# Performance work log

Hardware: AMD Instinct MI355X
Metric: run time of the kernel (lower is better)

## Reference

```python
import jax, jax.numpy as jnp
import numpy as np

NUM_USERS = 300_000
NUM_ITEMS = 200_000
N = NUM_USERS + NUM_ITEMS
DIM = 64
E = 2_500_000
NUM_LAYERS = 4
EMB_STD = 0.01


def setup_inputs() -> dict:
    key = jax.random.key(0)
    k1, k2, k3 = jax.random.split(key, 3)
    edge_index = jax.random.randint(k1, (2, E), 0, N, dtype=jnp.int32)
    emb_users = EMB_STD * jax.random.normal(k2, (NUM_USERS, DIM), dtype=jnp.float32)
    emb_items = EMB_STD * jax.random.normal(k3, (NUM_ITEMS, DIM), dtype=jnp.float32)
    return {"edge_index": edge_index, "emb_users": emb_users, "emb_items": emb_items}


def reference(edge_index, emb_users, emb_items):
    row, col = edge_index[0], edge_index[1]  # source, target
    x = jnp.concatenate([emb_users, emb_items], axis=0)  # [N, D]

    # gcn_norm (LGConv: no self loops): deg over target, sym normalization
    deg = jax.ops.segment_sum(jnp.ones((E,), x.dtype), col, num_segments=N)  # [N]
    deg_inv_sqrt = jnp.where(deg > 0, jax.lax.rsqrt(jnp.maximum(deg, 1.0)), 0.0)
    norm = deg_inv_sqrt[row] * deg_inv_sqrt[col]  # [E]

    embs = [x]
    for _ in range(NUM_LAYERS):
        # out[col] += norm * x[row]  (edge-wise gather, scale, scatter-add)
        x = jax.ops.segment_sum(norm[:, None] * x[row], col, num_segments=N)
        embs.append(x)

    # faithful to source: extra 1/(L+1) factor on top of the mean
    emb_final = (1.0 / (NUM_LAYERS + 1)) * jnp.mean(jnp.stack(embs, axis=1), axis=1)
    emb_users_final = emb_final[:NUM_USERS]
    emb_items_final = emb_final[NUM_USERS:]
    return (emb_users_final, emb_users, emb_items_final, emb_items)
```

## Files before the change

### kernel.cpp

```cpp
#include <hip/hip_runtime.h>
#include <stdint.h>

#define U_CNT 300000
#define I_CNT 200000
#define N_CNT 500000
#define DIM 64
#define SCAN_CHUNK 1024
#define NB1 ((N_CNT + SCAN_CHUNK - 1) / SCAN_CHUNK)

typedef unsigned short bf16_t;

__device__ __forceinline__ float lof(uint32_t u) { return __uint_as_float(u << 16); }
__device__ __forceinline__ float hif(uint32_t u) { return __uint_as_float(u & 0xFFFF0000u); }
__device__ __forceinline__ uint32_t rnd_bf(float f) {
    uint32_t u = __float_as_uint(f);
    return u + (0x7FFFu + ((u >> 16) & 1u));
}
__device__ __forceinline__ uint32_t packbf(float lo, float hi) {
    return (rnd_bf(lo) >> 16) | (rnd_bf(hi) & 0xFFFF0000u);
}
__device__ __forceinline__ bf16_t f2b(float f) { return (bf16_t)(rnd_bf(f) >> 16); }


__global__ void deg_cnt_kernel(const int* __restrict__ col, int* __restrict__ cnt, int E) {
    int e = blockIdx.x * blockDim.x + threadIdx.x;
    if (e < E) atomicAdd(&cnt[col[e]], 1);
}

__global__ void dis_kernel(const int* __restrict__ cnt, float* __restrict__ dis, int n) {
    int i = blockIdx.x * blockDim.x + threadIdx.x;
    if (i < n) {
        int d = cnt[i];
        dis[i] = d > 0 ? rsqrtf((float)d) : 0.0f;
    }
}


__global__ void scan1_kernel(const int* __restrict__ cnt, int* __restrict__ bsum, int n) {
    __shared__ int lds[256];
    int t = threadIdx.x;
    int i = blockIdx.x * SCAN_CHUNK + t * 4;
    int4 v = make_int4(0, 0, 0, 0);
    if (i + 3 < n) v = *(const int4*)(cnt + i);
    else {
        if (i     < n) v.x = cnt[i];
        if (i + 1 < n) v.y = cnt[i + 1];
        if (i + 2 < n) v.z = cnt[i + 2];
        if (i + 3 < n) v.w = cnt[i + 3];
    }
    lds[t] = v.x + v.y + v.z + v.w;
    __syncthreads();
    for (int o = 128; o > 0; o >>= 1) {
        if (t < o) lds[t] += lds[t + o];
        __syncthreads();
    }
    if (t == 0) bsum[blockIdx.x] = lds[0];
}

__global__ void scan2_kernel(int* __restrict__ bsum, int nb) {
    __shared__ int lds[512];
    int t = threadIdx.x;
    int v = (t < nb) ? bsum[t] : 0;
    lds[t] = v;
    __syncthreads();
    for (int o = 1; o < 512; o <<= 1) {
        int a = lds[t] + ((t >= o) ? lds[t - o] : 0);
        __syncthreads();
        lds[t] = a;
        __syncthreads();
    }
    if (t < nb) bsum[t] = lds[t] - v;
}

__global__ void scan3_kernel(const int* __restrict__ cnt, const int* __restrict__ bsum,
                             int* __restrict__ off, int* __restrict__ cur, int n, int E) {
    __shared__ int lds[256];
    int t = threadIdx.x;
    int i = blockIdx.x * SCAN_CHUNK + t * 4;
    int4 v = make_int4(0, 0, 0, 0);
    if (i + 3 < n) v = *(const int4*)(cnt + i);
    else {
        if (i     < n) v.x = cnt[i];
        if (i + 1 < n) v.y = cnt[i + 1];
        if (i + 2 < n) v.z = cnt[i + 2];
        if (i + 3 < n) v.w = cnt[i + 3];
    }
    int s = v.x + v.y + v.z + v.w;
    lds[t] = s;
    __syncthreads();
    for (int o = 1; o < 256; o <<= 1) {
        int a = lds[t] + ((t >= o) ? lds[t - o] : 0);
        __syncthreads();
        lds[t] = a;
        __syncthreads();
    }
    int ex = lds[t] - s + bsum[blockIdx.x];
    int o0 = ex, o1 = ex + v.x, o2 = o1 + v.y, o3 = o2 + v.z;
    if (i     < n) { off[i]     = o0; cur[i]     = o0; }
    if (i + 1 < n) { off[i + 1] = o1; cur[i + 1] = o1; }
    if (i + 2 < n) { off[i + 2] = o2; cur[i + 2] = o2; }
    if (i + 3 < n) { off[i + 3] = o3; cur[i + 3] = o3; }
    if (i == n - 4) off[n] = E;
}

__global__ void fill_kernel(const int* __restrict__ row, const int* __restrict__ col,
                            const float* __restrict__ dis, int* __restrict__ cur,
                            int2* __restrict__ csr, int E) {
    int e = blockIdx.x * blockDim.x + threadIdx.x;
    if (e < E) {
        int r = row[e], c = col[e];
        int p = atomicAdd(&cur[c], 1);
        int2 pr;
        pr.x = r;
        pr.y = __float_as_int(dis[r] * dis[c]);
        csr[p] = pr;
    }
}


__global__ void f2b_kernel(const float4* __restrict__ src, ushort4* __restrict__ dst, int n4) {
    int i = blockIdx.x * blockDim.x + threadIdx.x;
    if (i < n4) {
        float4 v = src[i];
        ushort4 w;
        w.x = f2b(v.x); w.y = f2b(v.y); w.z = f2b(v.z); w.w = f2b(v.w);
        dst[i] = w;
    }
}

__global__ __launch_bounds__(256) void gather8_kernel(
        const int* __restrict__ off, const int2* __restrict__ csr,
        const uint32_t* __restrict__ xb, uint4* __restrict__ yb, int nE) {
    int lane = threadIdx.x & 63;
    int sub  = lane & 7;
    int n = blockIdx.x * 32 + (threadIdx.x >> 6) * 8 + (lane >> 3);
    int s = off[n], e = off[n + 1];
    const uint4* xv = (const uint4*)xb;

    float a0 = 0, a1 = 0, a2 = 0, a3 = 0, a4 = 0, a5 = 0, a6 = 0, a7 = 0;

    int i0 = s;
    int2 pa = csr[(i0     < nE) ? i0     : (nE - 1)];
    int2 pb = csr[(i0 + 1 < nE) ? i0 + 1 : (nE - 1)];
    float na = (i0     < e) ? __int_as_float(pa.y) : 0.0f;
    float nb = (i0 + 1 < e) ? __int_as_float(pb.y) : 0.0f;
    int   ra = (i0     < e) ? pa.x : 0;
    int   rb = (i0 + 1 < e) ? pb.x : 0;
    uint4 va = xv[((size_t)ra << 3) + sub];
    uint4 vb = xv[((size_t)rb << 3) + sub];
    int i1 = i0 + 2;
    int2 qa = csr[(i1     < nE) ? i1     : (nE - 1)];
    int2 qb = csr[(i1 + 1 < nE) ? i1 + 1 : (nE - 1)];

    while (i0 < e) {
        float ma = (i1     < e) ? __int_as_float(qa.y) : 0.0f;
        float mb = (i1 + 1 < e) ? __int_as_float(qb.y) : 0.0f;
        int   sa = (i1     < e) ? qa.x : 0;
        int   sb = (i1 + 1 < e) ? qb.x : 0;
        uint4 wa = xv[((size_t)sa << 3) + sub];
        uint4 wb = xv[((size_t)sb << 3) + sub];
        int i2 = i1 + 2;
        qa = csr[(i2     < nE) ? i2     : (nE - 1)];
        qb = csr[(i2 + 1 < nE) ? i2 + 1 : (nE - 1)];
        a0 = fmaf(na, lof(va.x), a0); a1 = fmaf(na, hif(va.x), a1);
        a2 = fmaf(na, lof(va.y), a2); a3 = fmaf(na, hif(va.y), a3);
        a4 = fmaf(na, lof(va.z), a4); a5 = fmaf(na, hif(va.z), a5);
        a6 = fmaf(na, lof(va.w), a6); a7 = fmaf(na, hif(va.w), a7);
        a0 = fmaf(nb, lof(vb.x), a0); a1 = fmaf(nb, hif(vb.x), a1);
        a2 = fmaf(nb, lof(vb.y), a2); a3 = fmaf(nb, hif(vb.y), a3);
        a4 = fmaf(nb, lof(vb.z), a4); a5 = fmaf(nb, hif(vb.z), a5);
        a6 = fmaf(nb, lof(vb.w), a6); a7 = fmaf(nb, hif(vb.w), a7);
        va = wa; vb = wb; na = ma; nb = mb;
        i0 = i1; i1 = i2;
    }

    uint4 w;
    w.x = packbf(a0, a1); w.y = packbf(a2, a3);
    w.z = packbf(a4, a5); w.w = packbf(a6, a7);
    yb[((size_t)n << 3) + sub] = w;
}

__global__ __launch_bounds__(256) void gather_final_kernel(
        const int* __restrict__ off, const int2* __restrict__ csr,
        const uint32_t* __restrict__ xb,
        const uint4* __restrict__ y1, const uint4* __restrict__ y2,
        const float* __restrict__ embU, const float* __restrict__ embIadj,
        float* __restrict__ finU, float* __restrict__ finIadj,
        float* __restrict__ cpyU, float* __restrict__ cpyIadj, int nE) {
    int lane = threadIdx.x & 63;
    int sub  = lane & 7;
    int n = blockIdx.x * 32 + (threadIdx.x >> 6) * 8 + (lane >> 3);
    int s = off[n], e = off[n + 1];
    const uint4* xv = (const uint4*)xb;

    size_t nodeOff = ((size_t)n << 3) + sub;
    size_t fbase   = ((size_t)n << 6) + (size_t)sub * 8;
    const float* embP = (n < U_CNT ? embU : embIadj) + fbase;
    float*       finP = (n < U_CNT ? finU : finIadj) + fbase;
    float*       cpyP = (n < U_CNT ? cpyU : cpyIadj) + fbase;
    float4 b0 = *(const float4*)embP;
    float4 b1 = *(const float4*)(embP + 4);
    uint4 u1 = y1[nodeOff];
    uint4 u2 = y2[nodeOff];
    uint4 u3 = xv[nodeOff];

    float a0 = 0, a1 = 0, a2 = 0, a3 = 0, a4 = 0, a5 = 0, a6 = 0, a7 = 0;

    int i0 = s;
    int2 pa = csr[(i0     < nE) ? i0     : (nE - 1)];
    int2 pb = csr[(i0 + 1 < nE) ? i0 + 1 : (nE - 1)];
    float na = (i0     < e) ? __int_as_float(pa.y) : 0.0f;
    float nb = (i0 + 1 < e) ? __int_as_float(pb.y) : 0.0f;
    int   ra = (i0     < e) ? pa.x : 0;
    int   rb = (i0 + 1 < e) ? pb.x : 0;
    uint4 va = xv[((size_t)ra << 3) + sub];
    uint4 vb = xv[((size_t)rb << 3) + sub];
    int i1 = i0 + 2;
    int2 qa = csr[(i1     < nE) ? i1     : (nE - 1)];
    int2 qb = csr[(i1 + 1 < nE) ? i1 + 1 : (nE - 1)];

    while (i0 < e) {
        float ma = (i1     < e) ? __int_as_float(qa.y) : 0.0f;
        float mb = (i1 + 1 < e) ? __int_as_float(qb.y) : 0.0f;
        int   sa = (i1     < e) ? qa.x : 0;
        int   sb = (i1 + 1 < e) ? qb.x : 0;
        uint4 wa = xv[((size_t)sa << 3) + sub];
        uint4 wb = xv[((size_t)sb << 3) + sub];
        int i2 = i1 + 2;
        qa = csr[(i2     < nE) ? i2     : (nE - 1)];
        qb = csr[(i2 + 1 < nE) ? i2 + 1 : (nE - 1)];
        a0 = fmaf(na, lof(va.x), a0); a1 = fmaf(na, hif(va.x), a1);
        a2 = fmaf(na, lof(va.y), a2); a3 = fmaf(na, hif(va.y), a3);
        a4 = fmaf(na, lof(va.z), a4); a5 = fmaf(na, hif(va.z), a5);
        a6 = fmaf(na, lof(va.w), a6); a7 = fmaf(na, hif(va.w), a7);
        a0 = fmaf(nb, lof(vb.x), a0); a1 = fmaf(nb, hif(vb.x), a1);
        a2 = fmaf(nb, lof(vb.y), a2); a3 = fmaf(nb, hif(vb.y), a3);
        a4 = fmaf(nb, lof(vb.z), a4); a5 = fmaf(nb, hif(vb.z), a5);
        a6 = fmaf(nb, lof(vb.w), a6); a7 = fmaf(nb, hif(vb.w), a7);
        va = wa; vb = wb; na = ma; nb = mb;
        i0 = i1; i1 = i2;
    }

    const float k = 1.0f / 25.0f;
    float4 r0, r1;
    r0.x = (b0.x + lof(u1.x) + lof(u2.x) + lof(u3.x) + a0) * k;
    r0.y = (b0.y + hif(u1.x) + hif(u2.x) + hif(u3.x) + a1) * k;
    r0.z = (b0.z + lof(u1.y) + lof(u2.y) + lof(u3.y) + a2) * k;
    r0.w = (b0.w + hif(u1.y) + hif(u2.y) + hif(u3.y) + a3) * k;
    r1.x = (b1.x + lof(u1.z) + lof(u2.z) + lof(u3.z) + a4) * k;
    r1.y = (b1.y + hif(u1.z) + hif(u2.z) + hif(u3.z) + a5) * k;
    r1.z = (b1.z + lof(u1.w) + lof(u2.w) + lof(u3.w) + a6) * k;
    r1.w = (b1.w + hif(u1.w) + hif(u2.w) + hif(u3.w) + a7) * k;
    *(float4*)finP = r0;
    *(float4*)(finP + 4) = r1;
    *(float4*)cpyP = b0;
    *(float4*)(cpyP + 4) = b1;
}


extern "C" void kernel_launch(void* const* d_in, const int* in_sizes, int n_in,
                              void* d_out, int out_size, void* d_ws, size_t ws_size,
                              hipStream_t stream) {
    const int*   edge = (const int*)d_in[0];
    const float* embU = (const float*)d_in[1];
    const float* embI = (const float*)d_in[2];
    const int E = in_sizes[0] / 2;
    const int* row = edge;
    const int* col = edge + E;

    float* out  = (float*)d_out;
    float* finU = out;
    float* cu   = out + (size_t)U_CNT * DIM;
    float* finI = out + (size_t)2 * U_CNT * DIM;
    float* ci   = finI + (size_t)I_CNT * DIM;

    const size_t XB = (size_t)N_CNT * DIM * sizeof(bf16_t);
    char* ws = (char*)d_ws;
    size_t p = 0;
    bf16_t* x0 = (bf16_t*)(ws + p); p += XB;
    bf16_t* y1 = (bf16_t*)(ws + p); p += XB;
    bf16_t* y2 = (bf16_t*)(ws + p); p += XB;
    bf16_t* y3 = (bf16_t*)(ws + p); p += XB;
    int*   cnt  = (int*)(ws + p);   p += ((size_t)N_CNT + 4) * sizeof(int);
    int*   off  = (int*)(ws + p);   p += ((size_t)N_CNT + 4) * sizeof(int);
    int*   cur  = (int*)(ws + p);   p += ((size_t)N_CNT + 4) * sizeof(int);
    float* dis  = (float*)(ws + p); p += ((size_t)N_CNT + 4) * sizeof(float);
    int*   bsum = (int*)(ws + p);   p += 1024 * sizeof(int);
    int2*  csr  = (int2*)(ws + p);  p += (size_t)E * sizeof(int2);

    const float* embIadj = embI - (size_t)U_CNT * DIM;
    float* finIadj = finI - (size_t)U_CNT * DIM;
    float* ciadj   = ci   - (size_t)U_CNT * DIM;

    const int B = 256;
    const int nU4 = U_CNT * DIM / 4;
    const int nI4 = I_CNT * DIM / 4;
    const int gU4 = (nU4 + B - 1) / B;
    const int gI4 = (nI4 + B - 1) / B;
    const int gE  = (E + B - 1) / B;
    const int gN  = (N_CNT + B - 1) / B;
    const int gGather = N_CNT / 32;

    hipMemsetAsync(cnt, 0, (size_t)N_CNT * sizeof(int), stream);
    deg_cnt_kernel<<<gE, B, 0, stream>>>(col, cnt, E);
    dis_kernel<<<gN, B, 0, stream>>>(cnt, dis, N_CNT);

    scan1_kernel<<<NB1, 256, 0, stream>>>(cnt, bsum, N_CNT);
    scan2_kernel<<<1, 512, 0, stream>>>(bsum, NB1);
    scan3_kernel<<<NB1, 256, 0, stream>>>(cnt, bsum, off, cur, N_CNT, E);
    fill_kernel<<<gE, B, 0, stream>>>(row, col, dis, cur, csr, E);

    f2b_kernel<<<gU4, B, 0, stream>>>((const float4*)embU, (ushort4*)x0, nU4);
    f2b_kernel<<<gI4, B, 0, stream>>>((const float4*)embI,
                                      (ushort4*)(x0 + (size_t)U_CNT * DIM), nI4);

    gather8_kernel<<<gGather, B, 0, stream>>>(off, csr, (const uint32_t*)x0, (uint4*)y1, E);
    gather8_kernel<<<gGather, B, 0, stream>>>(off, csr, (const uint32_t*)y1, (uint4*)y2, E);
    gather8_kernel<<<gGather, B, 0, stream>>>(off, csr, (const uint32_t*)y2, (uint4*)y3, E);
    gather_final_kernel<<<gGather, B, 0, stream>>>(off, csr, (const uint32_t*)y3,
        (const uint4*)y1, (const uint4*)y2,
        embU, embIadj, finU, finIadj, cu, ciadj, E);
}
```

Baseline: 599.2 us.

## Factor symmetric norm into node scaling, shrink CSR to indices, fuse setup kernels

Rewrites propagation in pre-scaled form w = D^-1/2 x, so the edge list stores only source indices (4 B instead of 8 B per edge) and each layer applies a single per-node dis^2 scale after accumulation. The dis computation is folded into the scan kernel, and the CSR fill is merged with the bf16 conversion into one launch. The embedding copies are spread across the first two layer kernels, and the third layer writes a partial layer sum so the final kernel reads one buffer instead of three. The cost is an extra bf16 workspace buffer, extra rounding from storing scaled intermediates in bf16, and nontemporal loads and stores used throughout.

Measured after the change: 735.7 us. 1.23x slower.

```diff
diff --git a/kernel.cpp b/kernel.cpp
--- a/kernel.cpp
+++ b/kernel.cpp
@@ -9,6 +9,8 @@
 #define NB1 ((N_CNT + SCAN_CHUNK - 1) / SCAN_CHUNK)
 
 typedef unsigned short bf16_t;
+typedef float    f32x4 __attribute__((ext_vector_type(4)));
+typedef uint32_t u32x4 __attribute__((ext_vector_type(4)));
 
 __device__ __forceinline__ float lof(uint32_t u) { return __uint_as_float(u << 16); }
 __device__ __forceinline__ float hif(uint32_t u) { return __uint_as_float(u & 0xFFFF0000u); }
@@ -27,16 +29,10 @@
     if (e < E) atomicAdd(&cnt[col[e]], 1);
 }
 
-__global__ void dis_kernel(const int* __restrict__ cnt, float* __restrict__ dis, int n) {
-    int i = blockIdx.x * blockDim.x + threadIdx.x;
-    if (i < n) {
-        int d = cnt[i];
-        dis[i] = d > 0 ? rsqrtf((float)d) : 0.0f;
-    }
-}
-
-
-__global__ void scan1_kernel(const int* __restrict__ cnt, int* __restrict__ bsum, int n) {
+
+__global__ void scan1_dis_kernel(const int* __restrict__ cnt, int* __restrict__ bsum,
+                                 float* __restrict__ dis, float* __restrict__ dis2,
+                                 float* __restrict__ rdis, int n) {
     __shared__ int lds[256];
     int t = threadIdx.x;
     int i = blockIdx.x * SCAN_CHUNK + t * 4;
@@ -47,6 +43,25 @@
         if (i + 1 < n) v.y = cnt[i + 1];
         if (i + 2 < n) v.z = cnt[i + 2];
         if (i + 3 < n) v.w = cnt[i + 3];
+    }
+    if (i + 3 < n) {
+        int dd[4] = {v.x, v.y, v.z, v.w};
+        f32x4 fd, f2, fr;
+        #pragma unroll
+        for (int k = 0; k < 4; k++) {
+            float d = (float)dd[k];
+            float s = dd[k] > 0 ? rsqrtf(d) : 0.0f;
+            fd[k] = s; f2[k] = s * s; fr[k] = d * s;
+        }
+        *(f32x4*)(dis + i) = fd;
+        *(f32x4*)(dis2 + i) = f2;
+        *(f32x4*)(rdis + i) = fr;
+    } else {
+        for (int k = 0; k < 4 && i + k < n; k++) {
+            int d = (&v.x)[k];
+            float s = d > 0 ? rsqrtf((float)d) : 0.0f;
+            dis[i + k] = s; dis2[i + k] = s * s; rdis[i + k] = (float)d * s;
+        }
     }
     lds[t] = v.x + v.y + v.z + v.w;
     __syncthreads();
@@ -103,60 +118,78 @@
     if (i == n - 4) off[n] = E;
 }
 
-__global__ void fill_kernel(const int* __restrict__ row, const int* __restrict__ col,
-                            const float* __restrict__ dis, int* __restrict__ cur,
-                            int2* __restrict__ csr, int E) {
-    int e = blockIdx.x * blockDim.x + threadIdx.x;
-    if (e < E) {
-        int r = row[e], c = col[e];
-        int p = atomicAdd(&cur[c], 1);
-        int2 pr;
-        pr.x = r;
-        pr.y = __float_as_int(dis[r] * dis[c]);
-        csr[p] = pr;
-    }
-}
-
-
-__global__ void f2b_kernel(const float4* __restrict__ src, ushort4* __restrict__ dst, int n4) {
-    int i = blockIdx.x * blockDim.x + threadIdx.x;
-    if (i < n4) {
-        float4 v = src[i];
+
+__global__ void fill_w0_kernel(const int* __restrict__ row, const int* __restrict__ col,
+                               int* __restrict__ cur, int* __restrict__ csr, int E, int gE,
+                               const float* __restrict__ embU, const float* __restrict__ embIadj,
+                               const float* __restrict__ dis, ushort4* __restrict__ w0) {
+    int b = blockIdx.x;
+    if (b < gE) {
+        int e = b * blockDim.x + threadIdx.x;
+        if (e < E) {
+            int r = row[e], c = col[e];
+            int p = atomicAdd(&cur[c], 1);
+            csr[p] = r;
+        }
+    } else {
+        int q = (b - gE) * blockDim.x + threadIdx.x;
+        int node = q >> 4;
+        const float* src = (node < U_CNT ? embU : embIadj);
+        f32x4 v = __builtin_nontemporal_load((const f32x4*)src + q);
+        float dn = dis[node];
         ushort4 w;
-        w.x = f2b(v.x); w.y = f2b(v.y); w.z = f2b(v.z); w.w = f2b(v.w);
-        dst[i] = w;
-    }
-}
-
-__global__ __launch_bounds__(256) void gather8_kernel(
-        const int* __restrict__ off, const int2* __restrict__ csr,
-        const uint32_t* __restrict__ xb, uint4* __restrict__ yb, int nE) {
+        w.x = f2b(v[0] * dn); w.y = f2b(v[1] * dn);
+        w.z = f2b(v[2] * dn); w.w = f2b(v[3] * dn);
+        w0[q] = w;
+    }
+}
+
+__global__ __launch_bounds__(256) void gatherw_kernel(
+        const int* __restrict__ off, const int* __restrict__ csr,
+        const uint32_t* __restrict__ w_in, uint4* __restrict__ w_out,
+        const float* __restrict__ dis2, int nE,
+        u32x4* __restrict__ s_out, const u32x4* __restrict__ w1, const u32x4* __restrict__ w2,
+        const float* __restrict__ cpySrc, float* __restrict__ cpyDst, int cpyLo, int cpyHi) {
     int lane = threadIdx.x & 63;
     int sub  = lane & 7;
     int n = blockIdx.x * 32 + (threadIdx.x >> 6) * 8 + (lane >> 3);
     int s = off[n], e = off[n + 1];
-    const uint4* xv = (const uint4*)xb;
+    const uint4* xv = (const uint4*)w_in;
+    size_t nodeOff = ((size_t)n << 3) + sub;
+
+    u32x4 u1 = {0, 0, 0, 0}, u2 = {0, 0, 0, 0};
+    if (s_out) {
+        u1 = __builtin_nontemporal_load(w1 + nodeOff);
+        u2 = __builtin_nontemporal_load(w2 + nodeOff);
+    }
+    f32x4 cb0, cb1;
+    bool doCpy = (cpyDst != nullptr) && (n >= cpyLo) && (n < cpyHi);
+    size_t fbase = ((size_t)n << 6) + (size_t)sub * 8;
+    if (doCpy) {
+        cb0 = __builtin_nontemporal_load((const f32x4*)(cpySrc + fbase));
+        cb1 = __builtin_nontemporal_load((const f32x4*)(cpySrc + fbase + 4));
+    }
 
     float a0 = 0, a1 = 0, a2 = 0, a3 = 0, a4 = 0, a5 = 0, a6 = 0, a7 = 0;
 
     int i0 = s;
-    int2 pa = csr[(i0     < nE) ? i0     : (nE - 1)];
-    int2 pb = csr[(i0 + 1 < nE) ? i0 + 1 : (nE - 1)];
-    float na = (i0     < e) ? __int_as_float(pa.y) : 0.0f;
-    float nb = (i0 + 1 < e) ? __int_as_float(pb.y) : 0.0f;
-    int   ra = (i0     < e) ? pa.x : 0;
-    int   rb = (i0 + 1 < e) ? pb.x : 0;
+    int ca = csr[(i0     < nE) ? i0     : (nE - 1)];
+    int cb = csr[(i0 + 1 < nE) ? i0 + 1 : (nE - 1)];
+    float na = (i0     < e) ? 1.0f : 0.0f;
+    float nb = (i0 + 1 < e) ? 1.0f : 0.0f;
+    int   ra = (i0     < e) ? ca : 0;
+    int   rb = (i0 + 1 < e) ? cb : 0;
     uint4 va = xv[((size_t)ra << 3) + sub];
     uint4 vb = xv[((size_t)rb << 3) + sub];
     int i1 = i0 + 2;
-    int2 qa = csr[(i1     < nE) ? i1     : (nE - 1)];
-    int2 qb = csr[(i1 + 1 < nE) ? i1 + 1 : (nE - 1)];
+    int qa = csr[(i1     < nE) ? i1     : (nE - 1)];
+    int qb = csr[(i1 + 1 < nE) ? i1 + 1 : (nE - 1)];
 
     while (i0 < e) {
-        float ma = (i1     < e) ? __int_as_float(qa.y) : 0.0f;
-        float mb = (i1 + 1 < e) ? __int_as_float(qb.y) : 0.0f;
-        int   sa = (i1     < e) ? qa.x : 0;
-        int   sb = (i1 + 1 < e) ? qb.x : 0;
+        float ma = (i1     < e) ? 1.0f : 0.0f;
+        float mb = (i1 + 1 < e) ? 1.0f : 0.0f;
+        int   sa = (i1     < e) ? qa : 0;
+        int   sb = (i1 + 1 < e) ? qb : 0;
         uint4 wa = xv[((size_t)sa << 3) + sub];
         uint4 wb = xv[((size_t)sb << 3) + sub];
         int i2 = i1 + 2;
@@ -174,56 +207,70 @@
         i0 = i1; i1 = i2;
     }
 
+    float d2 = dis2[n];
+    a0 *= d2; a1 *= d2; a2 *= d2; a3 *= d2;
+    a4 *= d2; a5 *= d2; a6 *= d2; a7 *= d2;
+
     uint4 w;
     w.x = packbf(a0, a1); w.y = packbf(a2, a3);
     w.z = packbf(a4, a5); w.w = packbf(a6, a7);
-    yb[((size_t)n << 3) + sub] = w;
-}
-
-__global__ __launch_bounds__(256) void gather_final_kernel(
-        const int* __restrict__ off, const int2* __restrict__ csr,
-        const uint32_t* __restrict__ xb,
-        const uint4* __restrict__ y1, const uint4* __restrict__ y2,
+    w_out[nodeOff] = w;
+
+    if (s_out) {
+        u32x4 sv;
+        sv[0] = packbf(lof(u1[0]) + lof(u2[0]) + a0, hif(u1[0]) + hif(u2[0]) + a1);
+        sv[1] = packbf(lof(u1[1]) + lof(u2[1]) + a2, hif(u1[1]) + hif(u2[1]) + a3);
+        sv[2] = packbf(lof(u1[2]) + lof(u2[2]) + a4, hif(u1[2]) + hif(u2[2]) + a5);
+        sv[3] = packbf(lof(u1[3]) + lof(u2[3]) + a6, hif(u1[3]) + hif(u2[3]) + a7);
+        __builtin_nontemporal_store(sv, s_out + nodeOff);
+    }
+    if (doCpy) {
+        __builtin_nontemporal_store(cb0, (f32x4*)(cpyDst + fbase));
+        __builtin_nontemporal_store(cb1, (f32x4*)(cpyDst + fbase + 4));
+    }
+}
+
+
+__global__ __launch_bounds__(256) void final_kernel(
+        const int* __restrict__ off, const int* __restrict__ csr,
+        const uint32_t* __restrict__ w3, const u32x4* __restrict__ s3,
         const float* __restrict__ embU, const float* __restrict__ embIadj,
-        float* __restrict__ finU, float* __restrict__ finIadj,
-        float* __restrict__ cpyU, float* __restrict__ cpyIadj, int nE) {
+        const float* __restrict__ dis, const float* __restrict__ rdis,
+        float* __restrict__ finU, float* __restrict__ finIadj, int nE) {
     int lane = threadIdx.x & 63;
     int sub  = lane & 7;
     int n = blockIdx.x * 32 + (threadIdx.x >> 6) * 8 + (lane >> 3);
     int s = off[n], e = off[n + 1];
-    const uint4* xv = (const uint4*)xb;
-
+    const uint4* xv = (const uint4*)w3;
     size_t nodeOff = ((size_t)n << 3) + sub;
     size_t fbase   = ((size_t)n << 6) + (size_t)sub * 8;
+
     const float* embP = (n < U_CNT ? embU : embIadj) + fbase;
     float*       finP = (n < U_CNT ? finU : finIadj) + fbase;
-    float*       cpyP = (n < U_CNT ? cpyU : cpyIadj) + fbase;
-    float4 b0 = *(const float4*)embP;
-    float4 b1 = *(const float4*)(embP + 4);
-    uint4 u1 = y1[nodeOff];
-    uint4 u2 = y2[nodeOff];
-    uint4 u3 = xv[nodeOff];
+    f32x4 b0 = __builtin_nontemporal_load((const f32x4*)embP);
+    f32x4 b1 = __builtin_nontemporal_load((const f32x4*)(embP + 4));
+    u32x4 u3 = __builtin_nontemporal_load(s3 + nodeOff);
 
     float a0 = 0, a1 = 0, a2 = 0, a3 = 0, a4 = 0, a5 = 0, a6 = 0, a7 = 0;
 
     int i0 = s;
-    int2 pa = csr[(i0     < nE) ? i0     : (nE - 1)];
-    int2 pb = csr[(i0 + 1 < nE) ? i0 + 1 : (nE - 1)];
-    float na = (i0     < e) ? __int_as_float(pa.y) : 0.0f;
-    float nb = (i0 + 1 < e) ? __int_as_float(pb.y) : 0.0f;
-    int   ra = (i0     < e) ? pa.x : 0;
-    int   rb = (i0 + 1 < e) ? pb.x : 0;
+    int ca = csr[(i0     < nE) ? i0     : (nE - 1)];
+    int cb = csr[(i0 + 1 < nE) ? i0 + 1 : (nE - 1)];
+    float na = (i0     < e) ? 1.0f : 0.0f;
+    float nb = (i0 + 1 < e) ? 1.0f : 0.0f;
+    int   ra = (i0     < e) ? ca : 0;
+    int   rb = (i0 + 1 < e) ? cb : 0;
     uint4 va = xv[((size_t)ra << 3) + sub];
     uint4 vb = xv[((size_t)rb << 3) + sub];
     int i1 = i0 + 2;
-    int2 qa = csr[(i1     < nE) ? i1     : (nE - 1)];
-    int2 qb = csr[(i1 + 1 < nE) ? i1 + 1 : (nE - 1)];
+    int qa = csr[(i1     < nE) ? i1     : (nE - 1)];
+    int qb = csr[(i1 + 1 < nE) ? i1 + 1 : (nE - 1)];
 
     while (i0 < e) {
-        float ma = (i1     < e) ? __int_as_float(qa.y) : 0.0f;
-        float mb = (i1 + 1 < e) ? __int_as_float(qb.y) : 0.0f;
-        int   sa = (i1     < e) ? qa.x : 0;
-        int   sb = (i1 + 1 < e) ? qb.x : 0;
+        float ma = (i1     < e) ? 1.0f : 0.0f;
+        float mb = (i1 + 1 < e) ? 1.0f : 0.0f;
+        int   sa = (i1     < e) ? qa : 0;
+        int   sb = (i1 + 1 < e) ? qb : 0;
         uint4 wa = xv[((size_t)sa << 3) + sub];
         uint4 wb = xv[((size_t)sb << 3) + sub];
         int i2 = i1 + 2;
@@ -241,20 +288,20 @@
         i0 = i1; i1 = i2;
     }
 
+    float dn = dis[n];
+    float rd = rdis[n];
     const float k = 1.0f / 25.0f;
-    float4 r0, r1;
-    r0.x = (b0.x + lof(u1.x) + lof(u2.x) + lof(u3.x) + a0) * k;
-    r0.y = (b0.y + hif(u1.x) + hif(u2.x) + hif(u3.x) + a1) * k;
-    r0.z = (b0.z + lof(u1.y) + lof(u2.y) + lof(u3.y) + a2) * k;
-    r0.w = (b0.w + hif(u1.y) + hif(u2.y) + hif(u3.y) + a3) * k;
-    r1.x = (b1.x + lof(u1.z) + lof(u2.z) + lof(u3.z) + a4) * k;
-    r1.y = (b1.y + hif(u1.z) + hif(u2.z) + hif(u3.z) + a5) * k;
-    r1.z = (b1.z + lof(u1.w) + lof(u2.w) + lof(u3.w) + a6) * k;
-    r1.w = (b1.w + hif(u1.w) + hif(u2.w) + hif(u3.w) + a7) * k;
-    *(float4*)finP = r0;
-    *(float4*)(finP + 4) = r1;
-    *(float4*)cpyP = b0;
-    *(float4*)(cpyP + 4) = b1;
+    f32x4 r0, r1;
+    r0[0] = (b0[0] + rd * lof(u3[0]) + dn * a0) * k;
+    r0[1] = (b0[1] + rd * hif(u3[0]) + dn * a1) * k;
+    r0[2] = (b0[2] + rd * lof(u3[1]) + dn * a2) * k;
+    r0[3] = (b0[3] + rd * hif(u3[1]) + dn * a3) * k;
+    r1[0] = (b1[0] + rd * lof(u3[2]) + dn * a4) * k;
+    r1[1] = (b1[1] + rd * hif(u3[2]) + dn * a5) * k;
+    r1[2] = (b1[2] + rd * lof(u3[3]) + dn * a6) * k;
+    r1[3] = (b1[3] + rd * hif(u3[3]) + dn * a7) * k;
+    __builtin_nontemporal_store(r0, (f32x4*)finP);
+    __builtin_nontemporal_store(r1, (f32x4*)(finP + 4));
 }
 
 
@@ -277,47 +324,46 @@
     const size_t XB = (size_t)N_CNT * DIM * sizeof(bf16_t);
     char* ws = (char*)d_ws;
     size_t p = 0;
-    bf16_t* x0 = (bf16_t*)(ws + p); p += XB;
-    bf16_t* y1 = (bf16_t*)(ws + p); p += XB;
-    bf16_t* y2 = (bf16_t*)(ws + p); p += XB;
-    bf16_t* y3 = (bf16_t*)(ws + p); p += XB;
+    bf16_t* w0 = (bf16_t*)(ws + p); p += XB;
+    bf16_t* w1 = (bf16_t*)(ws + p); p += XB;
+    bf16_t* w2 = (bf16_t*)(ws + p); p += XB;
+    bf16_t* w3 = (bf16_t*)(ws + p); p += XB;
+    bf16_t* s3 = (bf16_t*)(ws + p); p += XB;
     int*   cnt  = (int*)(ws + p);   p += ((size_t)N_CNT + 4) * sizeof(int);
     int*   off  = (int*)(ws + p);   p += ((size_t)N_CNT + 4) * sizeof(int);
     int*   cur  = (int*)(ws + p);   p += ((size_t)N_CNT + 4) * sizeof(int);
     float* dis  = (float*)(ws + p); p += ((size_t)N_CNT + 4) * sizeof(float);
+    float* dis2 = (float*)(ws + p); p += ((size_t)N_CNT + 4) * sizeof(float);
+    float* rdis = (float*)(ws + p); p += ((size_t)N_CNT + 4) * sizeof(float);
     int*   bsum = (int*)(ws + p);   p += 1024 * sizeof(int);
-    int2*  csr  = (int2*)(ws + p);  p += (size_t)E * sizeof(int2);
+    int*   csr  = (int*)(ws + p);   p += (size_t)E * sizeof(int);
 
     const float* embIadj = embI - (size_t)U_CNT * DIM;
     float* finIadj = finI - (size_t)U_CNT * DIM;
     float* ciadj   = ci   - (size_t)U_CNT * DIM;
 
     const int B = 256;
-    const int nU4 = U_CNT * DIM / 4;
-    const int nI4 = I_CNT * DIM / 4;
-    const int gU4 = (nU4 + B - 1) / B;
-    const int gI4 = (nI4 + B - 1) / B;
     const int gE  = (E + B - 1) / B;
-    const int gN  = (N_CNT + B - 1) / B;
+    const int gW  = N_CNT * 16 / B;
     const int gGather = N_CNT / 32;
 
     hipMemsetAsync(cnt, 0, (size_t)N_CNT * sizeof(int), stream);
     deg_cnt_kernel<<<gE, B, 0, stream>>>(col, cnt, E);
-    dis_kernel<<<gN, B, 0, stream>>>(cnt, dis, N_CNT);
-
-    scan1_kernel<<<NB1, 256, 0, stream>>>(cnt, bsum, N_CNT);
+
+    scan1_dis_kernel<<<NB1, 256, 0, stream>>>(cnt, bsum, dis, dis2, rdis, N_CNT);
     scan2_kernel<<<1, 512, 0, stream>>>(bsum, NB1);
     scan3_kernel<<<NB1, 256, 0, stream>>>(cnt, bsum, off, cur, N_CNT, E);
-    fill_kernel<<<gE, B, 0, stream>>>(row, col, dis, cur, csr, E);
-
-    f2b_kernel<<<gU4, B, 0, stream>>>((const float4*)embU, (ushort4*)x0, nU4);
-    f2b_kernel<<<gI4, B, 0, stream>>>((const float4*)embI,
-                                      (ushort4*)(x0 + (size_t)U_CNT * DIM), nI4);
-
-    gather8_kernel<<<gGather, B, 0, stream>>>(off, csr, (const uint32_t*)x0, (uint4*)y1, E);
-    gather8_kernel<<<gGather, B, 0, stream>>>(off, csr, (const uint32_t*)y1, (uint4*)y2, E);
-    gather8_kernel<<<gGather, B, 0, stream>>>(off, csr, (const uint32_t*)y2, (uint4*)y3, E);
-    gather_final_kernel<<<gGather, B, 0, stream>>>(off, csr, (const uint32_t*)y3,
-        (const uint4*)y1, (const uint4*)y2,
-        embU, embIadj, finU, finIadj, cu, ciadj, E);
-}
+
+    fill_w0_kernel<<<gE + gW, B, 0, stream>>>(row, col, cur, csr, E, gE,
+                                              embU, embIadj, dis, (ushort4*)w0);
+
+    gatherw_kernel<<<gGather, B, 0, stream>>>(off, csr, (const uint32_t*)w0, (uint4*)w1,
+        dis2, E, nullptr, nullptr, nullptr, embU, cu, 0, U_CNT);
+    gatherw_kernel<<<gGather, B, 0, stream>>>(off, csr, (const uint32_t*)w1, (uint4*)w2,
+        dis2, E, nullptr, nullptr, nullptr, embIadj, ciadj, U_CNT, N_CNT);
+    gatherw_kernel<<<gGather, B, 0, stream>>>(off, csr, (const uint32_t*)w2, (uint4*)w3,
+        dis2, E, (u32x4*)s3, (const u32x4*)w1, (const u32x4*)w2, nullptr, nullptr, 0, 0);
+
+    final_kernel<<<gGather, B, 0, stream>>>(off, csr, (const uint32_t*)w3, (const u32x4*)s3,
+        embU, embIadj, dis, rdis, finU, finIadj, E);
+}
```
